# Performance work log

Measured on AMD Instinct MI355X. Metric: run time of the kernel, lower is better.

The kernel has to match this reference:

```python
import jax, jax.numpy as jnp
import numpy as np

# Allpass biquad coefficients (torchaudio.functional.allpass_biquad semantics)
SAMPLE_RATE = 16000
CENTRAL_FREQ = 4000.0
Q = 0.707

def _allpass_coeffs(sample_rate, central_freq, q):
    w0 = 2.0 * np.pi * central_freq / sample_rate
    alpha = np.sin(w0) / (2.0 * q)
    cos_w0 = np.cos(w0)
    b0 = 1.0 - alpha
    b1 = -2.0 * cos_w0
    b2 = 1.0 + alpha
    a0 = 1.0 + alpha
    a1 = -2.0 * cos_w0
    a2 = 1.0 - alpha
    # normalize by a0 (as torchaudio.biquad does)
    return (np.float32(b0 / a0), np.float32(b1 / a0), np.float32(b2 / a0),
            np.float32(a1 / a0), np.float32(a2 / a0))

B0, B1, B2, A1, A2 = _allpass_coeffs(SAMPLE_RATE, CENTRAL_FREQ, Q)


def setup_inputs() -> dict:
    key = jax.random.key(0)
    x = jax.random.normal(key, (64, 1, 480000), dtype=jnp.float32)
    return {"x": x}


def _biquad(x):
    # x: [B, 1, T] -> y: [B, 1, T]
    B, C, T = x.shape
    xt = jnp.transpose(x[:, 0, :])  # [T, B] for time-major scan

    def step(carry, xn):
        x1, x2, y1, y2 = carry
        yn = B0 * xn + B1 * x1 + B2 * x2 - A1 * y1 - A2 * y2
        return (xn, x1, yn, y1), yn

    z = jnp.zeros((B,), dtype=x.dtype)
    _, yt = jax.lax.scan(step, (z, z, z, z), xt)
    return jnp.transpose(yt)[:, None, :]  # back to [B, 1, T]


def reference(x):
    return _biquad(x)
```

## Files before the change

### kernel.cpp

```cpp
#include <hip/hip_runtime.h>
#include <cmath>

#define T_LEN   480000
#define BATCH   64
#define CHUNK   16
#define WARM    16
#define TPB     256
#define TS      (TPB * CHUNK)
#define TPR     ((T_LEN + TS - 1) / TS)
#define TPB_TILES 4
#define BPR     ((TPR + TPB_TILES - 1) / TPB_TILES)
#define NLOAD_MAX (TS + WARM)
#define NITER   ((NLOAD_MAX + TPB * 4 - 1) / (TPB * 4))
#define LDS_SLOTS (NLOAD_MAX + ((NLOAD_MAX >> 5) << 2))

__device__ __forceinline__ int slot4(int i) { return i + ((i >> 5) << 2); }

#define STEP(XN, YN)                                            \
    {                                                           \
        float u_ = fmaf(B0, (XN), fmaf(B1, x1, B2 * x2));       \
        (YN) = fmaf(-A1, y1, fmaf(-A2, y2, u_));                \
        x2 = x1; x1 = (XN); y2 = y1; y1 = (YN);                 \
    }

__global__ __launch_bounds__(TPB) void allpass_kernel(
    const float* __restrict__ x, float* __restrict__ y,
    float B0, float B1, float B2, float A1, float A2)
{
    __shared__ __align__(16) float lds[LDS_SLOTS];
    const int tid  = threadIdx.x;
    const int row  = blockIdx.x / BPR;
    const int tb0  = (blockIdx.x % BPR) * TPB_TILES;
    const int ntile = min(TPB_TILES, TPR - tb0);
    const float* __restrict__ xrow = x + (size_t)row * T_LEN;
    float* __restrict__ yrow       = y + (size_t)row * T_LEN;

    int sbase = tb0 * TS;
    int ns    = min(TS, T_LEN - sbase);
    int nload = ns + WARM;
    float4 vbuf[NITER];
    #pragma unroll
    for (int j = 0; j < NITER; ++j) {
        const int i4 = tid * 4 + j * (TPB * 4);
        if (i4 < nload) {
            if (tb0 == 0 && i4 < WARM)
                vbuf[j] = make_float4(0.f, 0.f, 0.f, 0.f);
            else
                vbuf[j] = *(const float4*)(xrow + sbase - WARM + i4);
        }
    }

    for (int it = 0; it < ntile; ++it) {
        #pragma unroll
        for (int j = 0; j < NITER; ++j) {
            const int i4 = tid * 4 + j * (TPB * 4);
            if (i4 < nload)
                *(float4*)&lds[slot4(i4)] = vbuf[j];
        }
        __syncthreads();

        const int cur_sbase = sbase, cur_ns = ns;

        if (it + 1 < ntile) {
            const int tb = tb0 + it + 1;
            sbase = tb * TS;
            ns    = min(TS, T_LEN - sbase);
            nload = ns + WARM;
            #pragma unroll
            for (int j = 0; j < NITER; ++j) {
                const int i4 = tid * 4 + j * (TPB * 4);
                if (i4 < nload)
                    vbuf[j] = *(const float4*)(xrow + sbase - WARM + i4);
            }
        }

        const int ls = tid * CHUNK;
        if (ls < cur_ns) {
            float x1 = 0.f, x2 = 0.f, y1 = 0.f, y2 = 0.f;
            #pragma unroll
            for (int t4 = 0; t4 < WARM; t4 += 4) {
                float4 xv = *(const float4*)&lds[slot4(ls + t4)];
                float t;
                STEP(xv.x, t); STEP(xv.y, t); STEP(xv.z, t); STEP(xv.w, t);
            }
            #pragma unroll
            for (int t4 = 0; t4 < CHUNK; t4 += 4) {
                float4 xv = *(const float4*)&lds[slot4(ls + WARM + t4)];
                float4 yv;
                STEP(xv.x, yv.x); STEP(xv.y, yv.y);
                STEP(xv.z, yv.z); STEP(xv.w, yv.w);
                *(float4*)(yrow + cur_sbase + ls + t4) = yv;
            }
        }
        __syncthreads();
    }
}

extern "C" void kernel_launch(void* const* d_in, const int* in_sizes, int n_in,
                              void* d_out, int out_size, void* d_ws, size_t ws_size,
                              hipStream_t stream) {
    const float* x = (const float*)d_in[0];
    float* y = (float*)d_out;

    const double sample_rate = 16000.0, central_freq = 4000.0, Q = 0.707;
    const double w0 = 2.0 * M_PI * central_freq / sample_rate;
    const double alpha = sin(w0) / (2.0 * Q);
    const double cw = cos(w0);
    const double a0 = 1.0 + alpha;
    const float B0 = (float)((1.0 - alpha) / a0);
    const float B1 = (float)((-2.0 * cw) / a0);
    const float B2 = (float)((1.0 + alpha) / a0);
    const float A1 = (float)((-2.0 * cw) / a0);
    const float A2 = (float)((1.0 - alpha) / a0);

    const int blocks = BATCH * BPR;
    allpass_kernel<<<blocks, TPB, 0, stream>>>(x, y, B0, B1, B2, A1, A2);
}
```

Before: 225.5 us.

## Stage outputs through LDS for coalesced nontemporal stores and nontemporal input loads

Each thread's 16 outputs are now kept in registers, written back into the LDS tile, and then stored to global memory with a coalesced, interleaved float4 pattern. Before, each thread wrote its own contiguous 64-byte chunk, so a wavefront's stores were strided. Input loads and output stores also use nontemporal builtins to avoid polluting the cache with streaming data. This adds two extra barriers and an LDS round trip per tile.

```diff
diff --git a/kernel.cpp b/kernel.cpp
--- a/kernel.cpp
+++ b/kernel.cpp
@@ -14,6 +14,8 @@
 #define NITER   ((NLOAD_MAX + TPB * 4 - 1) / (TPB * 4))
 #define LDS_SLOTS (NLOAD_MAX + ((NLOAD_MAX >> 5) << 2))
 
+typedef float f32x4 __attribute__((ext_vector_type(4)));
+
 __device__ __forceinline__ int slot4(int i) { return i + ((i >> 5) << 2); }
 
 #define STEP(XN, YN)                                            \
@@ -22,6 +24,7 @@
         (YN) = fmaf(-A1, y1, fmaf(-A2, y2, u_));                \
         x2 = x1; x1 = (XN); y2 = y1; y1 = (YN);                 \
     }
+
 
 __global__ __launch_bounds__(TPB) void allpass_kernel(
     const float* __restrict__ x, float* __restrict__ y,
@@ -38,15 +41,16 @@
     int sbase = tb0 * TS;
     int ns    = min(TS, T_LEN - sbase);
     int nload = ns + WARM;
-    float4 vbuf[NITER];
+    f32x4 vbuf[NITER];
     #pragma unroll
     for (int j = 0; j < NITER; ++j) {
         const int i4 = tid * 4 + j * (TPB * 4);
         if (i4 < nload) {
             if (tb0 == 0 && i4 < WARM)
-                vbuf[j] = make_float4(0.f, 0.f, 0.f, 0.f);
+                vbuf[j] = (f32x4){0.f, 0.f, 0.f, 0.f};
             else
-                vbuf[j] = *(const float4*)(xrow + sbase - WARM + i4);
+                vbuf[j] = __builtin_nontemporal_load(
+                              (const f32x4*)(xrow + sbase - WARM + i4));
         }
     }
 
@@ -55,7 +59,7 @@
         for (int j = 0; j < NITER; ++j) {
             const int i4 = tid * 4 + j * (TPB * 4);
             if (i4 < nload)
-                *(float4*)&lds[slot4(i4)] = vbuf[j];
+                *(f32x4*)&lds[slot4(i4)] = vbuf[j];
         }
         __syncthreads();
 
@@ -70,26 +74,46 @@
             for (int j = 0; j < NITER; ++j) {
                 const int i4 = tid * 4 + j * (TPB * 4);
                 if (i4 < nload)
-                    vbuf[j] = *(const float4*)(xrow + sbase - WARM + i4);
+                    vbuf[j] = __builtin_nontemporal_load(
+                                  (const f32x4*)(xrow + sbase - WARM + i4));
             }
         }
 
+        f32x4 yq[CHUNK / 4];
         const int ls = tid * CHUNK;
-        if (ls < cur_ns) {
+        const bool active = (ls < cur_ns);
+        if (active) {
             float x1 = 0.f, x2 = 0.f, y1 = 0.f, y2 = 0.f;
             #pragma unroll
             for (int t4 = 0; t4 < WARM; t4 += 4) {
-                float4 xv = *(const float4*)&lds[slot4(ls + t4)];
+                f32x4 xv = *(const f32x4*)&lds[slot4(ls + t4)];
                 float t;
                 STEP(xv.x, t); STEP(xv.y, t); STEP(xv.z, t); STEP(xv.w, t);
             }
             #pragma unroll
             for (int t4 = 0; t4 < CHUNK; t4 += 4) {
-                float4 xv = *(const float4*)&lds[slot4(ls + WARM + t4)];
-                float4 yv;
+                f32x4 xv = *(const f32x4*)&lds[slot4(ls + WARM + t4)];
+                f32x4 yv;
                 STEP(xv.x, yv.x); STEP(xv.y, yv.y);
                 STEP(xv.z, yv.z); STEP(xv.w, yv.w);
-                *(float4*)(yrow + cur_sbase + ls + t4) = yv;
+                yq[t4 / 4] = yv;
+            }
+        }
+        __syncthreads();
+
+        if (active) {
+            #pragma unroll
+            for (int t4 = 0; t4 < CHUNK; t4 += 4)
+                *(f32x4*)&lds[slot4(ls + t4)] = yq[t4 / 4];
+        }
+        __syncthreads();
+
+        #pragma unroll
+        for (int j = 0; j < NITER - 1; ++j) {
+            const int i4 = tid * 4 + j * (TPB * 4);
+            if (i4 < cur_ns) {
+                f32x4 v = *(const f32x4*)&lds[slot4(i4)];
+                __builtin_nontemporal_store(v, (f32x4*)(yrow + cur_sbase + i4));
             }
         }
         __syncthreads();
```

Result: faster. 207.3 us (-8.0%).
